# Optimization experiments

Measured on AMD Instinct MI355X. Metric: run time of the kernel, lower is better.

Reference implementation:

```python
import jax, jax.numpy as jnp
import numpy as np

IMAGES_PER_GPU = 2
IMAGE_MAX_DIM = 1024.0
POOL_SIZE = 7
NUM_ROIS = 1000


def crop_and_resize_level(fm0, boxes, pool_size):
    """TF-style crop_and_resize (bilinear, extrapolation_value=0).
    fm0: [C,H,W] feature map of image 0 (box_indices are all zero in the source).
    boxes: [N,4] normalized (y1,x1,y2,x2).
    returns crops: [N,C,pool_size,pool_size]
    """
    C, H, W = fm0.shape
    P = pool_size
    y1, x1, y2, x2 = boxes[:, 0], boxes[:, 1], boxes[:, 2], boxes[:, 3]
    t = jnp.arange(P, dtype=fm0.dtype) / (P - 1)  # [P]
    # sample coords in source pixel space: [N,P]
    ys = (y1[:, None] + t[None, :] * (y2 - y1)[:, None]) * (H - 1)
    xs = (x1[:, None] + t[None, :] * (x2 - x1)[:, None]) * (W - 1)
    valid_y = (ys >= 0) & (ys <= H - 1)
    valid_x = (xs >= 0) & (xs <= W - 1)
    ysc = jnp.clip(ys, 0.0, H - 1)
    xsc = jnp.clip(xs, 0.0, W - 1)
    y0 = jnp.floor(ysc).astype(jnp.int32)
    x0 = jnp.floor(xsc).astype(jnp.int32)
    y1i = jnp.minimum(y0 + 1, H - 1)
    x1i = jnp.minimum(x0 + 1, W - 1)
    ly = (ysc - y0)  # [N,P]
    lx = (xsc - x0)  # [N,P]

    def g(yi, xi):
        # advanced indexing broadcast -> [C,N,P,P]
        return fm0[:, yi[:, :, None], xi[:, None, :]]

    tl = g(y0, x0)
    tr = g(y0, x1i)
    bl = g(y1i, x0)
    br = g(y1i, x1i)
    lx_b = lx[None, :, None, :]
    ly_b = ly[None, :, :, None]
    top = tl + (tr - tl) * lx_b
    bot = bl + (br - bl) * lx_b
    out = top + (bot - top) * ly_b  # [C,N,P,P]
    mask = (valid_y[:, :, None] & valid_x[:, None, :])  # [N,P,P]
    out = out * mask[None].astype(out.dtype)
    return jnp.transpose(out, (1, 0, 2, 3))  # [N,C,P,P]


def roi_align(feature_maps, rois_flat, pool_size):
    """feature_maps: list of 4 arrays [B,256,Hl,Wl] for levels 2..5.
    rois_flat: [N,4] pixel coords (x1,y1,x2,y2). Returns [N,256,P,P]."""
    x1, y1, x2, y2 = rois_flat[:, 0], rois_flat[:, 1], rois_flat[:, 2], rois_flat[:, 3]
    area = (y2 - y1) * (x2 - x1)
    roi_level = jnp.log2(jnp.sqrt(jnp.maximum(area, 0.0)) / 224.0)
    roi_level = jnp.clip(jnp.round(roi_level) + 4, 2, 5)
    # boxes normalized and reordered (x1,y1,x2,y2) -> (y1,x1,y2,x2)
    boxes = rois_flat[:, jnp.array([1, 0, 3, 2])] / IMAGE_MAX_DIM
    N = rois_flat.shape[0]
    C = feature_maps[0].shape[1]
    pooled = jnp.zeros((N, C, pool_size, pool_size), dtype=feature_maps[0].dtype)
    for i, level in enumerate(range(2, 6)):
        crops = crop_and_resize_level(feature_maps[i][0], boxes, pool_size)
        sel = (roi_level == level)[:, None, None, None]
        pooled = jnp.where(sel, crops, pooled)
    return pooled


def setup_inputs() -> dict:
    key = jax.random.key(0)
    k2, k3, k4, k5, kxy, kwh = jax.random.split(key, 6)
    B, R = IMAGES_PER_GPU, NUM_ROIS
    p2 = jax.random.normal(k2, (B, 256, 256, 256), dtype=jnp.float32)
    p3 = jax.random.normal(k3, (B, 256, 128, 128), dtype=jnp.float32)
    p4 = jax.random.normal(k4, (B, 256, 64, 64), dtype=jnp.float32)
    p5 = jax.random.normal(k5, (B, 256, 32, 32), dtype=jnp.float32)
    xy1 = jax.random.uniform(kxy, (B, R, 2), minval=0.0, maxval=1000.0)
    wh = jax.random.uniform(kwh, (B, R, 2), minval=8.0, maxval=512.0)
    xy2 = jnp.clip(xy1 + wh, 0.0, IMAGE_MAX_DIM)
    rois = jnp.concatenate([xy1, xy2], axis=-1).astype(jnp.float32)  # (x1,y1,x2,y2)
    return {"p2": p2, "p3": p3, "p4": p4, "p5": p5, "rois": rois}


def reference(p2, p3, p4, p5, rois):
    B, R = rois.shape[0], rois.shape[1]
    rois_flat = rois.reshape(B * R, 4)
    pooled = roi_align([p2, p3, p4, p5], rois_flat, POOL_SIZE)
    return pooled.reshape(B, R, 256, POOL_SIZE, POOL_SIZE)
```

## Files before the change

### kernel.cpp

```cpp
#include <hip/hip_runtime.h>

#define P 7
#define PP 49
#define CMAX 256
#define G 8
#define CSPLIT 8
#define CSLICE 32
#define NBINS 256

#define WS_HIST   0
#define WS_CURSOR 256
#define WS_BUCKET 512
#define WS_PERM   2560

typedef float f2 __attribute__((ext_vector_type(2), aligned(4)));

struct PixParam { int o00, o10; float w00, w01, w10, w11; };

__device__ __forceinline__ int roi_level(float x1, float y1, float x2, float y2) {
    const float area = __fmul_rn(__fsub_rn(y2, y1), __fsub_rn(x2, x1));
    int lvl = (int)rintf(log2f(sqrtf(fmaxf(area, 0.0f)) / 224.0f)) + 4;
    return lvl < 2 ? 2 : (lvl > 5 ? 5 : lvl);
}

__global__ void zero_kernel(unsigned* ws) {
    ws[WS_HIST + threadIdx.x] = 0u;
}

__global__ void hist_kernel(const float* __restrict__ rois, int n, unsigned* ws) {
    const int r = blockIdx.x * blockDim.x + threadIdx.x;
    if (r >= n) return;
    const float x1 = rois[r*4+0], y1 = rois[r*4+1], x2 = rois[r*4+2], y2 = rois[r*4+3];
    const int lvl = roi_level(x1, y1, x2, y2);
    int cx = ((int)(__fmul_rn(__fadd_rn(x1, x2), 0.5f))) >> 7; cx = min(cx, 7);
    int cy = ((int)(__fmul_rn(__fadd_rn(y1, y2), 0.5f))) >> 7; cy = min(cy, 7);
    const int b = ((lvl - 2) << 6) | (cy << 3) | cx;
    ws[WS_BUCKET + r] = (unsigned)b;
    atomicAdd(&ws[WS_HIST + b], 1u);
}

__global__ void scan_kernel(unsigned* ws) {
    __shared__ unsigned s[NBINS];
    const int t = threadIdx.x;
    const unsigned h = ws[WS_HIST + t];
    s[t] = h;
    __syncthreads();
    for (int off = 1; off < NBINS; off <<= 1) {
        const unsigned v = (t >= off) ? s[t - off] : 0u;
        __syncthreads();
        s[t] += v;
        __syncthreads();
    }
    ws[WS_CURSOR + t] = s[t] - h;
}

__global__ void scatter_kernel(int n, unsigned* ws) {
    const int r = blockIdx.x * blockDim.x + threadIdx.x;
    if (r >= n) return;
    const unsigned b = ws[WS_BUCKET + r];
    const unsigned pos = atomicAdd(&ws[WS_CURSOR + b], 1u);
    ws[WS_PERM + pos] = (unsigned)r;
}

__global__ __launch_bounds__(256) void roialign_main(
    const float* __restrict__ p2, const float* __restrict__ p3,
    const float* __restrict__ p4, const float* __restrict__ p5,
    const float* __restrict__ rois, const unsigned* __restrict__ ws,
    float* __restrict__ out, int n)
{
    __shared__ PixParam sp[G * PP];
    __shared__ const float* fm_s[G];
    __shared__ int hw_s[G];
    __shared__ long long obase_s[G];

    const int nclust = (n + G - 1) / G;
    const int cl = blockIdx.x % nclust;
    const int cb = blockIdx.x / nclust;
    const int t  = threadIdx.x;

    for (int idx = t; idx < G * PP; idx += 256) {
        const int g = idx / PP, pix = idx % PP;
        const int gi = cl * G + g;
        PixParam pp; pp.o00 = 0; pp.o10 = 0;
        pp.w00 = 0.f; pp.w01 = 0.f; pp.w10 = 0.f; pp.w11 = 0.f;
        if (gi < n) {
            const int rr = (int)ws[WS_PERM + gi];
            const float x1 = rois[rr*4+0], y1 = rois[rr*4+1];
            const float x2 = rois[rr*4+2], y2 = rois[rr*4+3];
            const int lvl = roi_level(x1, y1, x2, y2);
            const int H = 1024 >> lvl;
            const float* fm = (lvl == 2) ? p2 : (lvl == 3) ? p3 : (lvl == 4) ? p4 : p5;

            const int py = pix / P, px = pix % P;
            const float inv = 1.0f / 1024.0f;
            const float by1 = __fmul_rn(y1, inv), bx1 = __fmul_rn(x1, inv);
            const float by2 = __fmul_rn(y2, inv), bx2 = __fmul_rn(x2, inv);
            const float Hm1 = (float)(H - 1);
            const float ty = (float)py / 6.0f;
            const float tx = (float)px / 6.0f;
            const float vy = __fmul_rn(__fadd_rn(by1, __fmul_rn(ty, __fsub_rn(by2, by1))), Hm1);
            const float vx = __fmul_rn(__fadd_rn(bx1, __fmul_rn(tx, __fsub_rn(bx2, bx1))), Hm1);
            const bool vldy = (vy >= 0.0f) && (vy <= Hm1);
            const bool vldx = (vx >= 0.0f) && (vx <= Hm1);
            const float yc = fminf(fmaxf(vy, 0.0f), Hm1);
            const float xc = fminf(fmaxf(vx, 0.0f), Hm1);
            const int y0 = (int)floorf(yc);
            const int x0 = (int)floorf(xc);
            const int y1i = min(y0 + 1, H - 1);
            const float ly = __fsub_rn(yc, (float)y0);
            const float lx = __fsub_rn(xc, (float)x0);
            const float m = (vldy && vldx) ? 1.0f : 0.0f;
            const float wy0 = m * (1.0f - ly), wy1 = m * ly;
            const float wx0 = 1.0f - lx,      wx1 = lx;
            pp.o00 = y0 * H + x0;
            pp.o10 = y1i * H + x0;
            pp.w00 = wy0 * wx0;  pp.w01 = wy0 * wx1;
            pp.w10 = wy1 * wx0;  pp.w11 = wy1 * wx1;
            if (pix == 0) {
                fm_s[g] = fm;
                hw_s[g] = H * H;
                obase_s[g] = (long long)rr * (CMAX * PP);
            }
        } else if (pix == 0) {
            fm_s[g] = p2; hw_s[g] = 0; obase_s[g] = -1;
        }
        sp[idx] = pp;
    }
    __syncthreads();

    if (t >= 5 * PP) return;
    const int pix = t % PP;
    const int c0  = t / PP;

    const float* pT[G]; const float* pB[G];
    size_t step[G];
    float w00[G], w01[G], w10[G], w11[G];
    long long ob[G];
    #pragma unroll
    for (int g = 0; g < G; ++g) {
        const PixParam pp = sp[g * PP + pix];
        const int hw = hw_s[g];
        const float* base = fm_s[g] + (size_t)(cb * CSLICE + c0) * hw;
        pT[g] = base + pp.o00;
        pB[g] = base + pp.o10;
        step[g] = (size_t)5 * hw;
        w00[g] = pp.w00; w01[g] = pp.w01; w10[g] = pp.w10; w11[g] = pp.w11;
        ob[g] = obase_s[g];
    }

    #pragma unroll
    for (int k = 0; k < 7; ++k) {
        const int clc = c0 + 5 * k;
        if (clc < CSLICE) {
            f2 tp[G], bt[G];
            #pragma unroll
            for (int g = 0; g < G; ++g) {
                tp[g] = *(const f2*)pT[g];
                bt[g] = *(const f2*)pB[g];
                pT[g] += step[g]; pB[g] += step[g];
            }
            #pragma unroll
            for (int g = 0; g < G; ++g) {
                const float v = tp[g].x * w00[g] + tp[g].y * w01[g]
                              + bt[g].x * w10[g] + bt[g].y * w11[g];
                if (ob[g] >= 0) {
                    out[ob[g] + (long long)(cb * CSLICE + clc) * PP + pix] = v;
                }
            }
        }
    }
}

extern "C" void kernel_launch(void* const* d_in, const int* in_sizes, int n_in,
                              void* d_out, int out_size, void* d_ws, size_t ws_size,
                              hipStream_t stream) {
    const float* p2   = (const float*)d_in[0];
    const float* p3   = (const float*)d_in[1];
    const float* p4   = (const float*)d_in[2];
    const float* p5   = (const float*)d_in[3];
    const float* rois = (const float*)d_in[4];
    float* out = (float*)d_out;
    unsigned* ws = (unsigned*)d_ws;
    const int n = in_sizes[4] / 4;

    const int nb = (n + 255) / 256;
    zero_kernel<<<1, NBINS, 0, stream>>>(ws);
    hist_kernel<<<nb, 256, 0, stream>>>(rois, n, ws);
    scan_kernel<<<1, NBINS, 0, stream>>>(ws);
    scatter_kernel<<<nb, 256, 0, stream>>>(n, ws);

    const int nclust = (n + G - 1) / G;
    roialign_main<<<nclust * CSPLIT, 256, 0, stream>>>(p2, p3, p4, p5, rois, ws, out, n);
}
```

Baseline: 301.1 us.

## Fuse bucketing prep into one kernel, remap blocks per XCD, halve channel slice

Folds the zero, histogram, scan and scatter passes into a single one-block prep kernel, which removes three launches and the global atomics. Each block of the main kernel now loads its ROI metadata once per group into shared memory instead of once per pixel. Block indices are remapped so that neighbouring clusters land on the same XCD, aimed at better L2 locality. CSPLIT goes from 8 to 16 for more blocks, and outputs are written with nontemporal stores. The single prep block handles at most 2048 ROIs (8 per thread), which matches this input but fixes a hard size limit.

```diff
diff --git a/kernel.cpp b/kernel.cpp
--- a/kernel.cpp
+++ b/kernel.cpp
@@ -4,13 +4,10 @@
 #define PP 49
 #define CMAX 256
 #define G 8
-#define CSPLIT 8
-#define CSLICE 32
+#define CSPLIT 16
+#define CSLICE 16
 #define NBINS 256
 
-#define WS_HIST   0
-#define WS_CURSOR 256
-#define WS_BUCKET 512
 #define WS_PERM   2560
 
 typedef float f2 __attribute__((ext_vector_type(2), aligned(4)));
@@ -23,43 +20,53 @@
     return lvl < 2 ? 2 : (lvl > 5 ? 5 : lvl);
 }
 
-__global__ void zero_kernel(unsigned* ws) {
-    ws[WS_HIST + threadIdx.x] = 0u;
-}
-
-__global__ void hist_kernel(const float* __restrict__ rois, int n, unsigned* ws) {
-    const int r = blockIdx.x * blockDim.x + threadIdx.x;
-    if (r >= n) return;
-    const float x1 = rois[r*4+0], y1 = rois[r*4+1], x2 = rois[r*4+2], y2 = rois[r*4+3];
-    const int lvl = roi_level(x1, y1, x2, y2);
-    int cx = ((int)(__fmul_rn(__fadd_rn(x1, x2), 0.5f))) >> 7; cx = min(cx, 7);
-    int cy = ((int)(__fmul_rn(__fadd_rn(y1, y2), 0.5f))) >> 7; cy = min(cy, 7);
-    const int b = ((lvl - 2) << 6) | (cy << 3) | cx;
-    ws[WS_BUCKET + r] = (unsigned)b;
-    atomicAdd(&ws[WS_HIST + b], 1u);
-}
-
-__global__ void scan_kernel(unsigned* ws) {
-    __shared__ unsigned s[NBINS];
+__global__ __launch_bounds__(256) void prep_kernel(
+    const float* __restrict__ rois, int n, unsigned* __restrict__ ws)
+{
+    __shared__ unsigned s_hist[NBINS];
+    __shared__ unsigned s_cur[NBINS];
     const int t = threadIdx.x;
-    const unsigned h = ws[WS_HIST + t];
-    s[t] = h;
+    s_hist[t] = 0u;
+    __syncthreads();
+
+    unsigned bloc[8];
+    #pragma unroll
+    for (int i = 0; i < 8; ++i) {
+        const int r = t + i * 256;
+        bloc[i] = 0u;
+        if (r < n) {
+            const float x1 = rois[r*4+0], y1 = rois[r*4+1];
+            const float x2 = rois[r*4+2], y2 = rois[r*4+3];
+            const int lvl = roi_level(x1, y1, x2, y2);
+            int cx = ((int)(__fmul_rn(__fadd_rn(x1, x2), 0.5f))) >> 7; cx = min(cx, 7);
+            int cy = ((int)(__fmul_rn(__fadd_rn(y1, y2), 0.5f))) >> 7; cy = min(cy, 7);
+            const unsigned b = (unsigned)(((lvl - 2) << 6) | (cy << 3) | cx);
+            bloc[i] = b;
+            atomicAdd(&s_hist[b], 1u);
+        }
+    }
+    __syncthreads();
+
+    const unsigned h = s_hist[t];
+    s_cur[t] = h;
     __syncthreads();
     for (int off = 1; off < NBINS; off <<= 1) {
-        const unsigned v = (t >= off) ? s[t - off] : 0u;
+        const unsigned v = (t >= off) ? s_cur[t - off] : 0u;
         __syncthreads();
-        s[t] += v;
+        s_cur[t] += v;
         __syncthreads();
     }
-    ws[WS_CURSOR + t] = s[t] - h;
-}
-
-__global__ void scatter_kernel(int n, unsigned* ws) {
-    const int r = blockIdx.x * blockDim.x + threadIdx.x;
-    if (r >= n) return;
-    const unsigned b = ws[WS_BUCKET + r];
-    const unsigned pos = atomicAdd(&ws[WS_CURSOR + b], 1u);
-    ws[WS_PERM + pos] = (unsigned)r;
+    s_cur[t] -= h;
+    __syncthreads();
+
+    #pragma unroll
+    for (int i = 0; i < 8; ++i) {
+        const int r = t + i * 256;
+        if (r < n) {
+            const unsigned pos = atomicAdd(&s_cur[bloc[i]], 1u);
+            ws[WS_PERM + pos] = (unsigned)r;
+        }
+    }
 }
 
 __global__ __launch_bounds__(256) void roialign_main(
@@ -71,26 +78,49 @@
     __shared__ PixParam sp[G * PP];
     __shared__ const float* fm_s[G];
     __shared__ int hw_s[G];
+    __shared__ int H_s[G];
     __shared__ long long obase_s[G];
+    __shared__ float box_s[G][4];
 
     const int nclust = (n + G - 1) / G;
-    const int cl = blockIdx.x % nclust;
-    const int cb = blockIdx.x / nclust;
+    const int nwg = nclust * CSPLIT;
+
+    const int pb  = blockIdx.x;
+    const int q   = nwg >> 3, rmd = nwg & 7;
+    const int xcd = pb & 7,   j   = pb >> 3;
+    const int l   = (xcd < rmd ? xcd * (q + 1) : rmd * (q + 1) + (xcd - rmd) * q) + j;
+
+    const int cl = l / CSPLIT;
+    const int cb = l % CSPLIT;
     const int t  = threadIdx.x;
+
+    if (t < G) {
+        const int gi = cl * G + t;
+        long long ob = -1; const float* fm = p2; int H = 4; int hw = 0;
+        float bx1 = 0.f, by1 = 0.f, bx2 = 0.f, by2 = 0.f;
+        if (gi < n) {
+            const int rr = (int)ws[WS_PERM + gi];
+            bx1 = rois[rr*4+0]; by1 = rois[rr*4+1];
+            bx2 = rois[rr*4+2]; by2 = rois[rr*4+3];
+            const int lvl = roi_level(bx1, by1, bx2, by2);
+            H = 1024 >> lvl;
+            hw = H * H;
+            fm = (lvl == 2) ? p2 : (lvl == 3) ? p3 : (lvl == 4) ? p4 : p5;
+            ob = (long long)rr * (CMAX * PP);
+        }
+        fm_s[t] = fm; hw_s[t] = hw; H_s[t] = H; obase_s[t] = ob;
+        box_s[t][0] = bx1; box_s[t][1] = by1; box_s[t][2] = bx2; box_s[t][3] = by2;
+    }
+    __syncthreads();
 
     for (int idx = t; idx < G * PP; idx += 256) {
         const int g = idx / PP, pix = idx % PP;
-        const int gi = cl * G + g;
         PixParam pp; pp.o00 = 0; pp.o10 = 0;
         pp.w00 = 0.f; pp.w01 = 0.f; pp.w10 = 0.f; pp.w11 = 0.f;
-        if (gi < n) {
-            const int rr = (int)ws[WS_PERM + gi];
-            const float x1 = rois[rr*4+0], y1 = rois[rr*4+1];
-            const float x2 = rois[rr*4+2], y2 = rois[rr*4+3];
-            const int lvl = roi_level(x1, y1, x2, y2);
-            const int H = 1024 >> lvl;
-            const float* fm = (lvl == 2) ? p2 : (lvl == 3) ? p3 : (lvl == 4) ? p4 : p5;
-
+        if (obase_s[g] >= 0) {
+            const float x1 = box_s[g][0], y1 = box_s[g][1];
+            const float x2 = box_s[g][2], y2 = box_s[g][3];
+            const int H = H_s[g];
             const int py = pix / P, px = pix % P;
             const float inv = 1.0f / 1024.0f;
             const float by1 = __fmul_rn(y1, inv), bx1 = __fmul_rn(x1, inv);
@@ -116,13 +146,6 @@
             pp.o10 = y1i * H + x0;
             pp.w00 = wy0 * wx0;  pp.w01 = wy0 * wx1;
             pp.w10 = wy1 * wx0;  pp.w11 = wy1 * wx1;
-            if (pix == 0) {
-                fm_s[g] = fm;
-                hw_s[g] = H * H;
-                obase_s[g] = (long long)rr * (CMAX * PP);
-            }
-        } else if (pix == 0) {
-            fm_s[g] = p2; hw_s[g] = 0; obase_s[g] = -1;
         }
         sp[idx] = pp;
     }
@@ -149,7 +172,7 @@
     }
 
     #pragma unroll
-    for (int k = 0; k < 7; ++k) {
+    for (int k = 0; k < 4; ++k) {
         const int clc = c0 + 5 * k;
         if (clc < CSLICE) {
             f2 tp[G], bt[G];
@@ -164,7 +187,8 @@
                 const float v = tp[g].x * w00[g] + tp[g].y * w01[g]
                               + bt[g].x * w10[g] + bt[g].y * w11[g];
                 if (ob[g] >= 0) {
-                    out[ob[g] + (long long)(cb * CSLICE + clc) * PP + pix] = v;
+                    __builtin_nontemporal_store(
+                        v, &out[ob[g] + (long long)(cb * CSLICE + clc) * PP + pix]);
                 }
             }
         }
@@ -183,11 +207,7 @@
     unsigned* ws = (unsigned*)d_ws;
     const int n = in_sizes[4] / 4;
 
-    const int nb = (n + 255) / 256;
-    zero_kernel<<<1, NBINS, 0, stream>>>(ws);
-    hist_kernel<<<nb, 256, 0, stream>>>(rois, n, ws);
-    scan_kernel<<<1, NBINS, 0, stream>>>(ws);
-    scatter_kernel<<<nb, 256, 0, stream>>>(n, ws);
+    prep_kernel<<<1, 256, 0, stream>>>(rois, n, ws);
 
     const int nclust = (n + G - 1) / G;
     roialign_main<<<nclust * CSPLIT, 256, 0, stream>>>(p2, p3, p4, p5, rois, ws, out, n);
```

Result: slower. 323.8 us (+7.5%).
